# Optimization experiments

Hardware: AMD Instinct MI355X
Metric: run time of the kernel (lower is better)

Reference implementation:

```python
import jax, jax.numpy as jnp
import numpy as np

BATCH, NUM_HEADS, SEQ, HEAD_DIM = 2, 32, 2048, 128
QMAX = 127.0  # symmetric int8 quantization range


def _fake_quant(x):
    # per-(head, token) symmetric int8 quantization + dequantization
    scale = jnp.max(jnp.abs(x), axis=-1, keepdims=True) / QMAX
    scale = jnp.maximum(scale, jnp.asarray(1e-8, x.dtype))
    q = jnp.clip(jnp.round(x / scale), -QMAX, QMAX)  # packed int8 values
    return q * scale  # dequantized


def setup_inputs() -> dict:
    key = jax.random.key(0)
    kq, kk, kv = jax.random.split(key, 3)
    shape = (BATCH, NUM_HEADS, SEQ, HEAD_DIM)
    return {
        "query": jax.random.normal(kq, shape, dtype=jnp.float32),
        "key": jax.random.normal(kk, shape, dtype=jnp.float32),
        "value": jax.random.normal(kv, shape, dtype=jnp.float32),
    }


def reference(query, key, value):
    # quantize K/V on the fly into the cache, then attend over dequantized K/V
    k_dq = _fake_quant(key)
    v_dq = _fake_quant(value)
    scale = jnp.asarray(1.0 / np.sqrt(HEAD_DIM), query.dtype)
    logits = jnp.einsum("bhqd,bhkd->bhqk", query, k_dq) * scale  # [B,H,Sq,Sk]
    weights = jax.nn.softmax(logits, axis=-1)
    out = jnp.einsum("bhqk,bhkd->bhqd", weights, v_dq)
    return out
```

## Files before the change

kernel.cpp:

```cpp
#include <hip/hip_runtime.h>
#include <hip/hip_bf16.h>

#define B 2
#define H 32
#define S 2048
#define D 128
#define NT 32

typedef __bf16 bf16x8 __attribute__((ext_vector_type(8)));
typedef float f32x4 __attribute__((ext_vector_type(4)));

union BF8U { unsigned int u[4]; unsigned short s[8]; bf16x8 b; int4 i4; };

static constexpr float INV_SQRT_D = 0.08838834764831845f;
static constexpr float LOG2E = 1.4426950408889634f;
static constexpr int NROWS = B * H * S;

__device__ __forceinline__ unsigned short bfbits(float f) {
    union { __bf16 h; unsigned short s; } cv;
    cv.h = (__bf16)f;
    return cv.s;
}
__device__ __forceinline__ unsigned int pack2bf(float a, float b) {
    union { unsigned short s[2]; unsigned int u; } cv;
    cv.s[0] = bfbits(a); cv.s[1] = bfbits(b);
    return cv.u;
}

typedef unsigned int u32;
__device__ __forceinline__ void async_ld16(const unsigned short* g, unsigned short* l) {
    __builtin_amdgcn_global_load_lds(
        (const __attribute__((address_space(1))) u32*)g,
        (__attribute__((address_space(3))) u32*)l, 16, 0, 0);
}

__global__ __launch_bounds__(256) void quant_k_kernel(
    const float* __restrict__ x, unsigned short* __restrict__ kpk,
    float* __restrict__ scl)
{
    const int row  = blockIdx.x * 4 + (threadIdx.x >> 6);
    const int lane = threadIdx.x & 63;
    const float2 v = *(const float2*)(x + (size_t)row * D + lane * 2);
    float m = fmaxf(fabsf(v.x), fabsf(v.y));
    #pragma unroll
    for (int off = 32; off; off >>= 1) m = fmaxf(m, __shfl_xor(m, off));
    const float scale = fmaxf(m / 127.0f, 1e-8f);
    const float q0 = fminf(fmaxf(rintf(v.x / scale), -127.0f), 127.0f);
    const float q1 = fminf(fmaxf(rintf(v.y / scale), -127.0f), 127.0f);
    const int bh = row >> 11, kv = row & 2047;
    const int t = kv >> 6, r = kv & 63, s = lane >> 2;
    unsigned short* dst = kpk + ((((size_t)bh * NT + t) * 16 + s) * 64 + r) * 8 + (lane & 3) * 2;
    *(unsigned int*)dst = pack2bf(q0, q1);
    if (lane == 0) scl[row] = scale * INV_SQRT_D * LOG2E;
}

__global__ __launch_bounds__(256) void quant_v_kernel(
    const float* __restrict__ x, unsigned short* __restrict__ vpk,
    float* __restrict__ scl)
{
    __shared__ __align__(16) unsigned short vt[D][72];
    const int bh = blockIdx.y;
    const int t  = blockIdx.x;
    const int s0 = t * 64;
    const int tid = threadIdx.x;
    const int wave = tid >> 6, lane = tid & 63;

    #pragma unroll 1
    for (int i = 0; i < 16; i++) {
        const int tok = wave * 16 + i;
        const float2 v = *(const float2*)(x + ((size_t)bh * S + s0 + tok) * D + lane * 2);
        float m = fmaxf(fabsf(v.x), fabsf(v.y));
        #pragma unroll
        for (int off = 32; off; off >>= 1) m = fmaxf(m, __shfl_xor(m, off));
        const float scale = fmaxf(m / 127.0f, 1e-8f);
        const float q0 = fminf(fmaxf(rintf(v.x / scale), -127.0f), 127.0f);
        const float q1 = fminf(fmaxf(rintf(v.y / scale), -127.0f), 127.0f);
        vt[lane * 2    ][tok] = bfbits(q0);
        vt[lane * 2 + 1][tok] = bfbits(q1);
        if (lane == 0) scl[(size_t)bh * S + s0 + tok] = scale;
    }
    __syncthreads();
    const int d = tid & 127, sh = tid >> 7;
    const size_t tb = ((size_t)bh * NT + t) * 8192;
    #pragma unroll
    for (int p = 0; p < 4; p++) {
        const int s = p * 2 + sh, kk = s >> 2, gg = s & 3;
        BF8U o;
        *(unsigned long long*)&o.s[0] = *(const unsigned long long*)&vt[d][32 * kk + 4 * gg];
        *(unsigned long long*)&o.s[4] = *(const unsigned long long*)&vt[d][32 * kk + 16 + 4 * gg];
        *(int4*)(vpk + tb + ((size_t)s * 128 + d) * 8) = o.i4;
    }
}

__global__ __launch_bounds__(256, 2) void attn_kernel(
    const float* __restrict__ Q, const unsigned short* __restrict__ Kpk,
    const float* __restrict__ Ksc, const unsigned short* __restrict__ Vpk,
    const float* __restrict__ Vsc, float* __restrict__ Out)
{
    __shared__ __align__(16) unsigned short Kb[2][8192];
    __shared__ __align__(16) unsigned short Vb[2][8192];

    const int wg = blockIdx.x;
    const int swz = (wg & 7) * 128 + (wg >> 3);
    const int bh = swz >> 4;
    const int qt = swz & 15;
    const int tid = threadIdx.x;
    const int wave = tid >> 6, lane = tid & 63;
    const int g = lane >> 4, c = lane & 15;

    const size_t tbase = (size_t)bh * NT * 8192;
    const size_t scb   = (size_t)bh * S;

    auto STAGE = [&](int tn, int pb) {
        const unsigned short* kt = Kpk + tbase + (size_t)tn * 8192;
        const unsigned short* vt = Vpk + tbase + (size_t)tn * 8192;
        #pragma unroll
        for (int i = 0; i < 4; i++) {
            const int ch = wave * 4 + i;
            async_ld16(kt + ch * 512 + lane * 8, &Kb[pb][ch * 512]);
            async_ld16(vt + ch * 512 + lane * 8, &Vb[pb][ch * 512]);
        }
    };

    bf16x8 qfA[4], qfB[4];
    {
        const float* qpA = Q + ((size_t)bh * S + qt * 128 + wave * 32 + c) * D + g * 8;
        const float* qpB = qpA + 16 * D;
        #pragma unroll
        for (int kk = 0; kk < 4; kk++) {
            float4 a = *(const float4*)(qpA + kk * 32);
            float4 b = *(const float4*)(qpA + kk * 32 + 4);
            BF8U t8;
            t8.s[0] = bfbits(a.x); t8.s[1] = bfbits(a.y); t8.s[2] = bfbits(a.z); t8.s[3] = bfbits(a.w);
            t8.s[4] = bfbits(b.x); t8.s[5] = bfbits(b.y); t8.s[6] = bfbits(b.z); t8.s[7] = bfbits(b.w);
            qfA[kk] = t8.b;
            a = *(const float4*)(qpB + kk * 32);
            b = *(const float4*)(qpB + kk * 32 + 4);
            t8.s[0] = bfbits(a.x); t8.s[1] = bfbits(a.y); t8.s[2] = bfbits(a.z); t8.s[3] = bfbits(a.w);
            t8.s[4] = bfbits(b.x); t8.s[5] = bfbits(b.y); t8.s[6] = bfbits(b.z); t8.s[7] = bfbits(b.w);
            qfB[kk] = t8.b;
        }
    }

    f32x4 accA[8], accB[8];
    const f32x4 zero = {0.f, 0.f, 0.f, 0.f};
    #pragma unroll
    for (int i = 0; i < 8; i++) { accA[i] = zero; accB[i] = zero; }
    float mA = -1e30f, lA = 0.f, mB = -1e30f, lB = 0.f;

    STAGE(0, 0);
    __syncthreads();

    #pragma unroll 1
    for (int t = 0; t < NT; t++) {
        const int cur = t & 1;
        if (t + 1 < NT) STAGE(t + 1, cur ^ 1);

        f32x4 sA[4], sB[4];
        __builtin_amdgcn_s_setprio(1);
        #pragma unroll
        for (int n = 0; n < 4; n++) {
            sA[n] = zero; sB[n] = zero;
            #pragma unroll
            for (int kk = 0; kk < 4; kk++) {
                bf16x8 kf = *(const bf16x8*)&Kb[cur][((4 * kk + g) * 64 + n * 16 + c) * 8];
                sA[n] = __builtin_amdgcn_mfma_f32_16x16x32_bf16(kf, qfA[kk], sA[n], 0, 0, 0);
                sB[n] = __builtin_amdgcn_mfma_f32_16x16x32_bf16(kf, qfB[kk], sB[n], 0, 0, 0);
            }
        }
        __builtin_amdgcn_s_setprio(0);

        const float* kscp = Ksc + scb + t * 64;
        float mxA = -1e30f, mxB = -1e30f;
        #pragma unroll
        for (int n = 0; n < 4; n++) {
            const f32x4 ks4 = *(const f32x4*)(kscp + n * 16 + 4 * g);
            #pragma unroll
            for (int j = 0; j < 4; j++) {
                sA[n][j] *= ks4[j];
                sB[n][j] *= ks4[j];
                mxA = fmaxf(mxA, sA[n][j]);
                mxB = fmaxf(mxB, sB[n][j]);
            }
        }
        mxA = fmaxf(mxA, __shfl_xor(mxA, 16));
        mxA = fmaxf(mxA, __shfl_xor(mxA, 32));
        mxB = fmaxf(mxB, __shfl_xor(mxB, 16));
        mxB = fmaxf(mxB, __shfl_xor(mxB, 32));

        if (!__all(mxA - mA <= 8.0f)) {
            const float mnew = fmaxf(mA, mxA);
            const float corr = exp2f(mA - mnew);
            mA = mnew; lA *= corr;
            float cq[4];
            #pragma unroll
            for (int r = 0; r < 4; r++) cq[r] = __shfl(corr, 4 * g + r);
            #pragma unroll
            for (int nd = 0; nd < 8; nd++)
                #pragma unroll
                for (int r = 0; r < 4; r++) accA[nd][r] *= cq[r];
        }
        if (!__all(mxB - mB <= 8.0f)) {
            const float mnew = fmaxf(mB, mxB);
            const float corr = exp2f(mB - mnew);
            mB = mnew; lB *= corr;
            float cq[4];
            #pragma unroll
            for (int r = 0; r < 4; r++) cq[r] = __shfl(corr, 4 * g + r);
            #pragma unroll
            for (int nd = 0; nd < 8; nd++)
                #pragma unroll
                for (int r = 0; r < 4; r++) accB[nd][r] *= cq[r];
        }

        const float* vscp = Vsc + scb + t * 64;
        float psA = 0.f, psB = 0.f;
        #pragma unroll
        for (int n = 0; n < 4; n++) {
            const f32x4 vs4 = *(const f32x4*)(vscp + n * 16 + 4 * g);
            #pragma unroll
            for (int j = 0; j < 4; j++) {
                float p = exp2f(sA[n][j] - mA);
                psA += p;
                sA[n][j] = p * vs4[j];
                p = exp2f(sB[n][j] - mB);
                psB += p;
                sB[n][j] = p * vs4[j];
            }
        }
        psA += __shfl_xor(psA, 16);
        psA += __shfl_xor(psA, 32);
        lA += psA;
        psB += __shfl_xor(psB, 16);
        psB += __shfl_xor(psB, 32);
        lB += psB;

        __builtin_amdgcn_s_setprio(1);
        #pragma unroll
        for (int kk = 0; kk < 2; kk++) {
            BF8U a8, b8;
            a8.u[0] = pack2bf(sA[2 * kk][0], sA[2 * kk][1]);
            a8.u[1] = pack2bf(sA[2 * kk][2], sA[2 * kk][3]);
            a8.u[2] = pack2bf(sA[2 * kk + 1][0], sA[2 * kk + 1][1]);
            a8.u[3] = pack2bf(sA[2 * kk + 1][2], sA[2 * kk + 1][3]);
            b8.u[0] = pack2bf(sB[2 * kk][0], sB[2 * kk][1]);
            b8.u[1] = pack2bf(sB[2 * kk][2], sB[2 * kk][3]);
            b8.u[2] = pack2bf(sB[2 * kk + 1][0], sB[2 * kk + 1][1]);
            b8.u[3] = pack2bf(sB[2 * kk + 1][2], sB[2 * kk + 1][3]);
            const bf16x8 pfA = a8.b, pfB = b8.b;
            #pragma unroll
            for (int nd = 0; nd < 8; nd++) {
                bf16x8 vf = *(const bf16x8*)&Vb[cur][((kk * 4 + g) * 128 + nd * 16 + c) * 8];
                accA[nd] = __builtin_amdgcn_mfma_f32_16x16x32_bf16(pfA, vf, accA[nd], 0, 0, 0);
                accB[nd] = __builtin_amdgcn_mfma_f32_16x16x32_bf16(pfB, vf, accB[nd], 0, 0, 0);
            }
        }
        __builtin_amdgcn_s_setprio(0);

        __syncthreads();
    }

    const float invA = 1.0f / lA, invB = 1.0f / lB;
    float iqA[4], iqB[4];
    #pragma unroll
    for (int r = 0; r < 4; r++) {
        iqA[r] = __shfl(invA, 4 * g + r);
        iqB[r] = __shfl(invB, 4 * g + r);
    }
    const size_t obase = ((size_t)bh * S + qt * 128 + wave * 32) * (size_t)D;
    #pragma unroll
    for (int r = 0; r < 4; r++) {
        const int q = 4 * g + r;
        #pragma unroll
        for (int nd = 0; nd < 8; nd++) {
            Out[obase + (size_t)q * D + nd * 16 + c] = accA[nd][r] * iqA[r];
            Out[obase + (size_t)(q + 16) * D + nd * 16 + c] = accB[nd][r] * iqB[r];
        }
    }
}

extern "C" void kernel_launch(void* const* d_in, const int* in_sizes, int n_in,
                              void* d_out, int out_size, void* d_ws, size_t ws_size,
                              hipStream_t stream) {
    const float* q = (const float*)d_in[0];
    const float* k = (const float*)d_in[1];
    const float* v = (const float*)d_in[2];
    float* out = (float*)d_out;

    const size_t ELEMS = (size_t)NROWS * D;
    unsigned short* kpk = (unsigned short*)d_ws;
    unsigned short* vpk = kpk + ELEMS;
    float* ks = (float*)(vpk + ELEMS);
    float* vs = ks + NROWS;

    quant_k_kernel<<<NROWS / 4, 256, 0, stream>>>(k, kpk, ks);
    quant_v_kernel<<<dim3(NT, B * H), 256, 0, stream>>>(v, vpk, vs);
    attn_kernel<<<1024, 256, 0, stream>>>(q, kpk, ks, vpk, vs, out);
}
```

Baseline: 285.0 us.

## Halve KV tile to 32 tokens, raise occupancy, fold V scale into bf16 values

Shrinks the attention KV tile from 64 to 32 tokens, which halves the shared-memory buffers, and raises launch bounds to three workgroups per CU so more waves can hide latency. V is now stored pre-dequantized in bf16 (q*scale), which removes the per-tile V scale loads and multiplies in the softmax stage. The cost is twice as many loop iterations, so barriers, max/rescale checks and shuffles run twice as often. Rounding the dequantized V to bf16 differs slightly from rounding the integer codes exactly.

```diff
diff --git a/kernel.cpp b/kernel.cpp
--- a/kernel.cpp
+++ b/kernel.cpp
@@ -5,7 +5,8 @@
 #define H 32
 #define S 2048
 #define D 128
-#define NT 32
+#define KVB 32
+#define NT 64
 
 typedef __bf16 bf16x8 __attribute__((ext_vector_type(8)));
 typedef float f32x4 __attribute__((ext_vector_type(4)));
@@ -48,20 +49,19 @@
     const float q0 = fminf(fmaxf(rintf(v.x / scale), -127.0f), 127.0f);
     const float q1 = fminf(fmaxf(rintf(v.y / scale), -127.0f), 127.0f);
     const int bh = row >> 11, kv = row & 2047;
-    const int t = kv >> 6, r = kv & 63, s = lane >> 2;
-    unsigned short* dst = kpk + ((((size_t)bh * NT + t) * 16 + s) * 64 + r) * 8 + (lane & 3) * 2;
+    const int t = kv >> 5, r = kv & 31, s = lane >> 2;
+    unsigned short* dst = kpk + ((((size_t)bh * NT + t) * 16 + s) * KVB + r) * 8 + (lane & 3) * 2;
     *(unsigned int*)dst = pack2bf(q0, q1);
     if (lane == 0) scl[row] = scale * INV_SQRT_D * LOG2E;
 }
 
 __global__ __launch_bounds__(256) void quant_v_kernel(
-    const float* __restrict__ x, unsigned short* __restrict__ vpk,
-    float* __restrict__ scl)
+    const float* __restrict__ x, unsigned short* __restrict__ vpk)
 {
     __shared__ __align__(16) unsigned short vt[D][72];
     const int bh = blockIdx.y;
-    const int t  = blockIdx.x;
-    const int s0 = t * 64;
+    const int tb2 = blockIdx.x;
+    const int s0 = tb2 * 64;
     const int tid = threadIdx.x;
     const int wave = tid >> 6, lane = tid & 63;
 
@@ -75,30 +75,29 @@
         const float scale = fmaxf(m / 127.0f, 1e-8f);
         const float q0 = fminf(fmaxf(rintf(v.x / scale), -127.0f), 127.0f);
         const float q1 = fminf(fmaxf(rintf(v.y / scale), -127.0f), 127.0f);
-        vt[lane * 2    ][tok] = bfbits(q0);
-        vt[lane * 2 + 1][tok] = bfbits(q1);
-        if (lane == 0) scl[(size_t)bh * S + s0 + tok] = scale;
+        vt[lane * 2    ][tok] = bfbits(q0 * scale);
+        vt[lane * 2 + 1][tok] = bfbits(q1 * scale);
     }
     __syncthreads();
     const int d = tid & 127, sh = tid >> 7;
-    const size_t tb = ((size_t)bh * NT + t) * 8192;
     #pragma unroll
     for (int p = 0; p < 4; p++) {
-        const int s = p * 2 + sh, kk = s >> 2, gg = s & 3;
+        const int sl = p * 2 + sh;
+        const int h = sl >> 2, g = sl & 3;
         BF8U o;
-        *(unsigned long long*)&o.s[0] = *(const unsigned long long*)&vt[d][32 * kk + 4 * gg];
-        *(unsigned long long*)&o.s[4] = *(const unsigned long long*)&vt[d][32 * kk + 16 + 4 * gg];
-        *(int4*)(vpk + tb + ((size_t)s * 128 + d) * 8) = o.i4;
-    }
-}
-
-__global__ __launch_bounds__(256, 2) void attn_kernel(
+        *(unsigned long long*)&o.s[0] = *(const unsigned long long*)&vt[d][h * 32 + 4 * g];
+        *(unsigned long long*)&o.s[4] = *(const unsigned long long*)&vt[d][h * 32 + 16 + 4 * g];
+        *(int4*)(vpk + ((((size_t)bh * NT + tb2 * 2 + h) * 4 + g) * 128 + d) * 8) = o.i4;
+    }
+}
+
+__global__ __launch_bounds__(256, 3) void attn_kernel(
     const float* __restrict__ Q, const unsigned short* __restrict__ Kpk,
     const float* __restrict__ Ksc, const unsigned short* __restrict__ Vpk,
-    const float* __restrict__ Vsc, float* __restrict__ Out)
+    float* __restrict__ Out)
 {
-    __shared__ __align__(16) unsigned short Kb[2][8192];
-    __shared__ __align__(16) unsigned short Vb[2][8192];
+    __shared__ __align__(16) unsigned short Kb[2][4096];
+    __shared__ __align__(16) unsigned short Vb[2][4096];
 
     const int wg = blockIdx.x;
     const int swz = (wg & 7) * 128 + (wg >> 3);
@@ -108,15 +107,15 @@
     const int wave = tid >> 6, lane = tid & 63;
     const int g = lane >> 4, c = lane & 15;
 
-    const size_t tbase = (size_t)bh * NT * 8192;
+    const size_t tbase = (size_t)bh * NT * 4096;
     const size_t scb   = (size_t)bh * S;
 
     auto STAGE = [&](int tn, int pb) {
-        const unsigned short* kt = Kpk + tbase + (size_t)tn * 8192;
-        const unsigned short* vt = Vpk + tbase + (size_t)tn * 8192;
-        #pragma unroll
-        for (int i = 0; i < 4; i++) {
-            const int ch = wave * 4 + i;
+        const unsigned short* kt = Kpk + tbase + (size_t)tn * 4096;
+        const unsigned short* vt = Vpk + tbase + (size_t)tn * 4096;
+        #pragma unroll
+        for (int i = 0; i < 2; i++) {
+            const int ch = wave * 2 + i;
             async_ld16(kt + ch * 512 + lane * 8, &Kb[pb][ch * 512]);
             async_ld16(vt + ch * 512 + lane * 8, &Vb[pb][ch * 512]);
         }
@@ -156,24 +155,24 @@
         const int cur = t & 1;
         if (t + 1 < NT) STAGE(t + 1, cur ^ 1);
 
-        f32x4 sA[4], sB[4];
+        f32x4 sA[2], sB[2];
         __builtin_amdgcn_s_setprio(1);
         #pragma unroll
-        for (int n = 0; n < 4; n++) {
+        for (int n = 0; n < 2; n++) {
             sA[n] = zero; sB[n] = zero;
             #pragma unroll
             for (int kk = 0; kk < 4; kk++) {
-                bf16x8 kf = *(const bf16x8*)&Kb[cur][((4 * kk + g) * 64 + n * 16 + c) * 8];
+                bf16x8 kf = *(const bf16x8*)&Kb[cur][((4 * kk + g) * KVB + n * 16 + c) * 8];
                 sA[n] = __builtin_amdgcn_mfma_f32_16x16x32_bf16(kf, qfA[kk], sA[n], 0, 0, 0);
                 sB[n] = __builtin_amdgcn_mfma_f32_16x16x32_bf16(kf, qfB[kk], sB[n], 0, 0, 0);
             }
         }
         __builtin_amdgcn_s_setprio(0);
 
-        const float* kscp = Ksc + scb + t * 64;
+        const float* kscp = Ksc + scb + t * KVB;
         float mxA = -1e30f, mxB = -1e30f;
         #pragma unroll
-        for (int n = 0; n < 4; n++) {
+        for (int n = 0; n < 2; n++) {
             const f32x4 ks4 = *(const f32x4*)(kscp + n * 16 + 4 * g);
             #pragma unroll
             for (int j = 0; j < 4; j++) {
@@ -213,19 +212,17 @@
                 for (int r = 0; r < 4; r++) accB[nd][r] *= cq[r];
         }
 
-        const float* vscp = Vsc + scb + t * 64;
         float psA = 0.f, psB = 0.f;
         #pragma unroll
-        for (int n = 0; n < 4; n++) {
-            const f32x4 vs4 = *(const f32x4*)(vscp + n * 16 + 4 * g);
+        for (int n = 0; n < 2; n++) {
             #pragma unroll
             for (int j = 0; j < 4; j++) {
                 float p = exp2f(sA[n][j] - mA);
                 psA += p;
-                sA[n][j] = p * vs4[j];
+                sA[n][j] = p;
                 p = exp2f(sB[n][j] - mB);
                 psB += p;
-                sB[n][j] = p * vs4[j];
+                sB[n][j] = p;
             }
         }
         psA += __shfl_xor(psA, 16);
@@ -236,21 +233,20 @@
         lB += psB;
 
         __builtin_amdgcn_s_setprio(1);
-        #pragma unroll
-        for (int kk = 0; kk < 2; kk++) {
+        {
             BF8U a8, b8;
-            a8.u[0] = pack2bf(sA[2 * kk][0], sA[2 * kk][1]);
-            a8.u[1] = pack2bf(sA[2 * kk][2], sA[2 * kk][3]);
-            a8.u[2] = pack2bf(sA[2 * kk + 1][0], sA[2 * kk + 1][1]);
-            a8.u[3] = pack2bf(sA[2 * kk + 1][2], sA[2 * kk + 1][3]);
-            b8.u[0] = pack2bf(sB[2 * kk][0], sB[2 * kk][1]);
-            b8.u[1] = pack2bf(sB[2 * kk][2], sB[2 * kk][3]);
-            b8.u[2] = pack2bf(sB[2 * kk + 1][0], sB[2 * kk + 1][1]);
-            b8.u[3] = pack2bf(sB[2 * kk + 1][2], sB[2 * kk + 1][3]);
+            a8.u[0] = pack2bf(sA[0][0], sA[0][1]);
+            a8.u[1] = pack2bf(sA[0][2], sA[0][3]);
+            a8.u[2] = pack2bf(sA[1][0], sA[1][1]);
+            a8.u[3] = pack2bf(sA[1][2], sA[1][3]);
+            b8.u[0] = pack2bf(sB[0][0], sB[0][1]);
+            b8.u[1] = pack2bf(sB[0][2], sB[0][3]);
+            b8.u[2] = pack2bf(sB[1][0], sB[1][1]);
+            b8.u[3] = pack2bf(sB[1][2], sB[1][3]);
             const bf16x8 pfA = a8.b, pfB = b8.b;
             #pragma unroll
             for (int nd = 0; nd < 8; nd++) {
-                bf16x8 vf = *(const bf16x8*)&Vb[cur][((kk * 4 + g) * 128 + nd * 16 + c) * 8];
+                bf16x8 vf = *(const bf16x8*)&Vb[cur][(g * 128 + nd * 16 + c) * 8];
                 accA[nd] = __builtin_amdgcn_mfma_f32_16x16x32_bf16(pfA, vf, accA[nd], 0, 0, 0);
                 accB[nd] = __builtin_amdgcn_mfma_f32_16x16x32_bf16(pfB, vf, accB[nd], 0, 0, 0);
             }
@@ -291,9 +287,8 @@
     unsigned short* kpk = (unsigned short*)d_ws;
     unsigned short* vpk = kpk + ELEMS;
     float* ks = (float*)(vpk + ELEMS);
-    float* vs = ks + NROWS;
 
     quant_k_kernel<<<NROWS / 4, 256, 0, stream>>>(k, kpk, ks);
-    quant_v_kernel<<<dim3(NT, B * H), 256, 0, stream>>>(v, vpk, vs);
-    attn_kernel<<<1024, 256, 0, stream>>>(q, kpk, ks, vpk, vs, out);
-}
+    quant_v_kernel<<<dim3(S / 64, B * H), 256, 0, stream>>>(v, vpk);
+    attn_kernel<<<1024, 256, 0, stream>>>(q, kpk, ks, vpk, out);
+}
```

Result: slower. 293.2 us (+2.9%).

## Pre-dequantize V into bf16 and load V fragments directly from global

Applied to the files above, without the earlier changes.

V is now stored as dequantized bf16 (q*scale) in the quant kernel, so the per-token V scale buffer and the multiply in the softmax loop go away. The attention kernel stops staging V through LDS and instead loads V fragments straight from global/L2 into registers at the start of each tile, halving LDS use. This cuts shared-memory traffic and the V scale multiply, but adds register pressure (16 bf16x8 fragments) and exposes global-load latency that the LDS double-buffering previously hid. Rounding q*scale to bf16 differs slightly from the earlier split representation.

```diff
diff --git a/kernel.cpp b/kernel.cpp
--- a/kernel.cpp
+++ b/kernel.cpp
@@ -55,8 +55,7 @@
 }
 
 __global__ __launch_bounds__(256) void quant_v_kernel(
-    const float* __restrict__ x, unsigned short* __restrict__ vpk,
-    float* __restrict__ scl)
+    const float* __restrict__ x, unsigned short* __restrict__ vpk)
 {
     __shared__ __align__(16) unsigned short vt[D][72];
     const int bh = blockIdx.y;
@@ -75,9 +74,8 @@
         const float scale = fmaxf(m / 127.0f, 1e-8f);
         const float q0 = fminf(fmaxf(rintf(v.x / scale), -127.0f), 127.0f);
         const float q1 = fminf(fmaxf(rintf(v.y / scale), -127.0f), 127.0f);
-        vt[lane * 2    ][tok] = bfbits(q0);
-        vt[lane * 2 + 1][tok] = bfbits(q1);
-        if (lane == 0) scl[(size_t)bh * S + s0 + tok] = scale;
+        vt[lane * 2    ][tok] = bfbits(q0 * scale);
+        vt[lane * 2 + 1][tok] = bfbits(q1 * scale);
     }
     __syncthreads();
     const int d = tid & 127, sh = tid >> 7;
@@ -95,10 +93,9 @@
 __global__ __launch_bounds__(256, 2) void attn_kernel(
     const float* __restrict__ Q, const unsigned short* __restrict__ Kpk,
     const float* __restrict__ Ksc, const unsigned short* __restrict__ Vpk,
-    const float* __restrict__ Vsc, float* __restrict__ Out)
+    float* __restrict__ Out)
 {
     __shared__ __align__(16) unsigned short Kb[2][8192];
-    __shared__ __align__(16) unsigned short Vb[2][8192];
 
     const int wg = blockIdx.x;
     const int swz = (wg & 7) * 128 + (wg >> 3);
@@ -113,12 +110,10 @@
 
     auto STAGE = [&](int tn, int pb) {
         const unsigned short* kt = Kpk + tbase + (size_t)tn * 8192;
-        const unsigned short* vt = Vpk + tbase + (size_t)tn * 8192;
         #pragma unroll
         for (int i = 0; i < 4; i++) {
             const int ch = wave * 4 + i;
             async_ld16(kt + ch * 512 + lane * 8, &Kb[pb][ch * 512]);
-            async_ld16(vt + ch * 512 + lane * 8, &Vb[pb][ch * 512]);
         }
     };
 
@@ -170,6 +165,14 @@
         }
         __builtin_amdgcn_s_setprio(0);
 
+        const unsigned short* vtg = Vpk + tbase + (size_t)t * 8192;
+        bf16x8 vf[2][8];
+        #pragma unroll
+        for (int kk = 0; kk < 2; kk++)
+            #pragma unroll
+            for (int nd = 0; nd < 8; nd++)
+                vf[kk][nd] = *(const bf16x8*)(vtg + ((kk * 4 + g) * 128 + nd * 16 + c) * 8);
+
         const float* kscp = Ksc + scb + t * 64;
         float mxA = -1e30f, mxB = -1e30f;
         #pragma unroll
@@ -213,19 +216,17 @@
                 for (int r = 0; r < 4; r++) accB[nd][r] *= cq[r];
         }
 
-        const float* vscp = Vsc + scb + t * 64;
         float psA = 0.f, psB = 0.f;
         #pragma unroll
         for (int n = 0; n < 4; n++) {
-            const f32x4 vs4 = *(const f32x4*)(vscp + n * 16 + 4 * g);
             #pragma unroll
             for (int j = 0; j < 4; j++) {
                 float p = exp2f(sA[n][j] - mA);
                 psA += p;
-                sA[n][j] = p * vs4[j];
+                sA[n][j] = p;
                 p = exp2f(sB[n][j] - mB);
                 psB += p;
-                sB[n][j] = p * vs4[j];
+                sB[n][j] = p;
             }
         }
         psA += __shfl_xor(psA, 16);
@@ -250,9 +251,8 @@
             const bf16x8 pfA = a8.b, pfB = b8.b;
             #pragma unroll
             for (int nd = 0; nd < 8; nd++) {
-                bf16x8 vf = *(const bf16x8*)&Vb[cur][((kk * 4 + g) * 128 + nd * 16 + c) * 8];
-                accA[nd] = __builtin_amdgcn_mfma_f32_16x16x32_bf16(pfA, vf, accA[nd], 0, 0, 0);
-                accB[nd] = __builtin_amdgcn_mfma_f32_16x16x32_bf16(pfB, vf, accB[nd], 0, 0, 0);
+                accA[nd] = __builtin_amdgcn_mfma_f32_16x16x32_bf16(pfA, vf[kk][nd], accA[nd], 0, 0, 0);
+                accB[nd] = __builtin_amdgcn_mfma_f32_16x16x32_bf16(pfB, vf[kk][nd], accB[nd], 0, 0, 0);
             }
         }
         __builtin_amdgcn_s_setprio(0);
@@ -291,9 +291,8 @@
     unsigned short* kpk = (unsigned short*)d_ws;
     unsigned short* vpk = kpk + ELEMS;
     float* ks = (float*)(vpk + ELEMS);
-    float* vs = ks + NROWS;
 
     quant_k_kernel<<<NROWS / 4, 256, 0, stream>>>(k, kpk, ks);
-    quant_v_kernel<<<dim3(NT, B * H), 256, 0, stream>>>(v, vpk, vs);
-    attn_kernel<<<1024, 256, 0, stream>>>(q, kpk, ks, vpk, vs, out);
-}
+    quant_v_kernel<<<dim3(NT, B * H), 256, 0, stream>>>(v, vpk);
+    attn_kernel<<<1024, 256, 0, stream>>>(q, kpk, ks, vpk, out);
+}
```

Result: no change. 285.5 us (+0.2%).
